# Kernel tuning notes

Measured on AMD Instinct MI355X. Metric: run time of the kernel, lower is better.

The kernel has to match this reference:

```python
import jax, jax.numpy as jnp
import numpy as np
from jax import lax

B, Hs, Ws = 2, 256, 256
DIM = 256        # query channels (c)
DIM_BAK = 256    # key/value channels (c2)
HEADS = 8
WIN = 8
HEAD_DIM = DIM // HEADS
SCALE = HEAD_DIM ** -0.5


def window_partition(x, ws):
    # x: [B, H, W, C] -> [B*nH*nW, ws, ws, C]
    b, h, w, c = x.shape
    x = x.reshape(b, h // ws, ws, w // ws, ws, c)
    return x.transpose(0, 1, 3, 2, 4, 5).reshape(-1, ws, ws, c)


def window_reverse(windows, ws, h, w):
    # windows: [B*nH*nW, ws, ws, C] -> [B, H, W, C]
    b = windows.shape[0] // ((h // ws) * (w // ws))
    x = windows.reshape(b, h // ws, w // ws, ws, ws, -1)
    return x.transpose(0, 1, 3, 2, 4, 5).reshape(b, h, w, -1)


def setup_inputs() -> dict:
    key = jax.random.key(0)
    ks = jax.random.split(key, 9)
    s = 0.02
    return {
        "query_feature": jax.random.normal(ks[0], (B, DIM, Hs, Ws), jnp.float32),
        "key_value_feature": jax.random.normal(ks[1], (B, DIM_BAK, Hs, Ws), jnp.float32),
        # depthwise 3x3 conv on kv (groups=DIM_BAK, bias=False): OIHW with I=1
        "w_dw": jax.random.normal(ks[2], (DIM_BAK, 1, 3, 3), jnp.float32) * s,
        # to_q: Linear(dim -> dim), stored [in, out]
        "wq": jax.random.normal(ks[3], (DIM, DIM), jnp.float32) * s,
        "bq": jax.random.normal(ks[4], (DIM,), jnp.float32) * s,
        # to_kv: Linear(dim_bak -> 2*dim)
        "wkv": jax.random.normal(ks[5], (DIM_BAK, 2 * DIM), jnp.float32) * s,
        "bkv": jax.random.normal(ks[6], (2 * DIM,), jnp.float32) * s,
        # project_out: Linear(dim -> dim)
        "w_proj": jax.random.normal(ks[7], (DIM, DIM), jnp.float32) * s,
        "b_proj": jax.random.normal(ks[8], (DIM,), jnp.float32) * s,
    }


def reference(query_feature, key_value_feature, w_dw, wq, bq, wkv, bkv, w_proj, b_proj):
    b, c, h, w = query_feature.shape
    c2 = key_value_feature.shape[1]

    # depthwise 3x3 conv on key/value feature (padding=1, stride=1)
    kv = lax.conv_general_dilated(
        key_value_feature, w_dw,
        window_strides=(1, 1), padding="SAME",
        feature_group_count=c2,
        dimension_numbers=("NCHW", "OIHW", "NCHW"))

    # NCHW -> NHWC, partition into non-overlapping windows
    qw = window_partition(query_feature.transpose(0, 2, 3, 1), WIN)  # [B_, ws, ws, c]
    kvw = window_partition(kv.transpose(0, 2, 3, 1), WIN)            # [B_, ws, ws, c2]
    B_ = qw.shape[0]
    N = WIN * WIN
    qw = qw.reshape(B_, N, c)
    kvw = kvw.reshape(B_, N, c2)

    # projections -> multi-head [B_, heads, N, head_dim]
    q = (qw @ wq + bq).reshape(B_, N, HEADS, HEAD_DIM).transpose(0, 2, 1, 3) * SCALE
    kv_proj = (kvw @ wkv + bkv).reshape(B_, N, 2, HEADS, HEAD_DIM)
    k = kv_proj[:, :, 0].transpose(0, 2, 1, 3)
    v = kv_proj[:, :, 1].transpose(0, 2, 1, 3)

    # windowed cross-attention
    attn = jax.nn.softmax(jnp.einsum("bhnd,bhmd->bhnm", q, k), axis=-1)
    out = jnp.einsum("bhnm,bhmd->bhnd", attn, v)
    out = out.transpose(0, 2, 1, 3).reshape(B_, N, c)
    out = out @ w_proj + b_proj

    # reverse windows, back to NCHW
    out = window_reverse(out.reshape(B_, WIN, WIN, c), WIN, h, w)
    return out.transpose(0, 3, 1, 2)
```

## Files before the change

### kernel.cpp

```cpp
#include <hip/hip_runtime.h>
#include <hip/hip_bf16.h>
#include <cstdint>
#include <cstddef>

typedef __hip_bfloat16 bf16;
typedef short bf16x8 __attribute__((ext_vector_type(8)));
typedef float f32x4 __attribute__((ext_vector_type(4)));

#define MFMA(a, b, c) __builtin_amdgcn_mfma_f32_16x16x32_bf16((a), (b), (c), 0, 0, 0)

__global__ __launch_bounds__(256) void wtrans_k(const float* __restrict__ wq,
                                                const float* __restrict__ wkv,
                                                const float* __restrict__ wp,
                                                bf16* __restrict__ wqT,
                                                bf16* __restrict__ wkvT,
                                                bf16* __restrict__ wpT) {
  int idx = blockIdx.x * 256 + threadIdx.x;
  if (idx < 65536) {
    int n = idx >> 8, k = idx & 255;
    wqT[idx] = __float2bfloat16(wq[k * 256 + n]);
  } else if (idx < 196608) {
    int i = idx - 65536;
    int n = i >> 8, k = i & 255;
    wkvT[i] = __float2bfloat16(wkv[k * 512 + n]);
  } else {
    int i = idx - 196608;
    int n = i >> 8, k = i & 255;
    wpT[i] = __float2bfloat16(wp[k * 256 + n]);
  }
}

__global__ __launch_bounds__(256) void t_winq_k(const float* __restrict__ src,
                                                bf16* __restrict__ dst,
                                                int hw0, int swoff) {
  __shared__ bf16 T[64][66];
  int tile = blockIdx.x;
  int c0 = (tile & 3) << 6;
  int hwb = hw0 + ((tile >> 2) << 6);
  int tid = threadIdx.x;
  {
    int hwl = tid & 63, cb = tid >> 6;
    const float* s = src + (size_t)(c0 + cb) * 65536 + hwb + hwl;
#pragma unroll
    for (int i = 0; i < 16; ++i)
      T[cb + i * 4][hwl] = __float2bfloat16(s[(size_t)i * 4 * 65536]);
  }
  __syncthreads();
  {
    int cl = tid & 63, hb = tid >> 6;
#pragma unroll
    for (int j = 0; j < 16; ++j) {
      int hwl = hb + j * 4;
      int hw = hwb + hwl;
      int h = hw >> 8, w = hw & 255;
      int sw = swoff + ((h >> 3) << 5) + (w >> 3);
      int t = ((h & 7) << 3) + (w & 7);
      dst[((size_t)(sw * 64 + t) << 8) + c0 + cl] = T[cl][hwl];
    }
  }
}

__global__ __launch_bounds__(256) void t_nhwc_k(const float* __restrict__ src,
                                                bf16* __restrict__ dst) {
  __shared__ bf16 T[64][66];
  int tile = blockIdx.x;
  int c0 = (tile & 3) << 6;
  int hwoff = (tile >> 2) << 6;
  int tid = threadIdx.x;
  {
    int hwl = tid & 63, cb = tid >> 6;
    const float* s = src + (size_t)(c0 + cb) * 65536 + hwoff + hwl;
#pragma unroll
    for (int i = 0; i < 16; ++i)
      T[cb + i * 4][hwl] = __float2bfloat16(s[(size_t)i * 4 * 65536]);
  }
  __syncthreads();
  {
    int cl = tid & 63, hb = tid >> 6;
#pragma unroll
    for (int j = 0; j < 16; ++j) {
      int hwl = hb + j * 4;
      dst[((size_t)(hwoff + hwl) << 8) + c0 + cl] = T[cl][hwl];
    }
  }
}

__global__ __launch_bounds__(256) void convkv_k(const bf16* __restrict__ SK,
                                                const float* __restrict__ wdw,
                                                const bf16* __restrict__ wkvT,
                                                const float* __restrict__ bkv,
                                                bf16* __restrict__ k_s,
                                                bf16* __restrict__ vT_s,
                                                int wid_base, int cnt, int psw0,
                                                int nwtot) {
  __shared__ __align__(16) bf16 X[64 * 256];
  auto xp = [&](int row, int col) -> bf16* {
    int by = (row << 9) + (col << 1);
    by ^= (row & 7) << 4;
    return (bf16*)((char*)X + by);
  };
  int bid = blockIdx.x;
  int swc = (bid & 7) * (cnt >> 3) + (bid >> 3);
  int sw = psw0 + swc;
  int wid = wid_base + swc;
  int rem = wid & 1023, wh = rem >> 5, ww = rem & 31;
  int h0 = wh * 8, w0 = ww * 8;
  int tid = threadIdx.x;
  {
    int c = tid;
    float wr[9];
#pragma unroll
    for (int q = 0; q < 9; ++q) wr[q] = wdw[c * 9 + q];
    const bool wlo = (w0 > 0), whi = (w0 < 248);
    float rows[3][10];
    auto load_row = [&](int gh, float* r) {
      if (gh >= 0 && gh < 256) {
        const bf16* rp = SK + ((size_t)(gh * 256 + w0) << 8) + c;
        r[0] = wlo ? __bfloat162float(rp[-256]) : 0.f;
#pragma unroll
        for (int s = 1; s <= 8; ++s) r[s] = __bfloat162float(rp[(s - 1) * 256]);
        r[9] = whi ? __bfloat162float(rp[8 * 256]) : 0.f;
      } else {
#pragma unroll
        for (int e = 0; e < 10; ++e) r[e] = 0.f;
      }
    };
    load_row(h0 - 1, rows[0]);
    load_row(h0, rows[1]);
#pragma unroll
    for (int i = 0; i < 8; ++i) {
      load_row(h0 + i + 1, rows[(i + 2) % 3]);
#pragma unroll
      for (int j = 0; j < 8; ++j) {
        float acc = 0.f;
#pragma unroll
        for (int di = 0; di < 3; ++di) {
          const float* rp = rows[(i + di) % 3];
          acc = __builtin_fmaf(wr[di * 3 + 0], rp[j], acc);
          acc = __builtin_fmaf(wr[di * 3 + 1], rp[j + 1], acc);
          acc = __builtin_fmaf(wr[di * 3 + 2], rp[j + 2], acc);
        }
        *xp(i * 8 + j, c) = __float2bfloat16(acc);
      }
    }
  }
  __syncthreads();
  int wave = tid >> 6, lane = tid & 63, quad = lane >> 4, l16 = lane & 15;
  int n0 = wave * 64;
  f32x4 zero4 = {0.f, 0.f, 0.f, 0.f};
  f32x4 acc[4][4];
  for (int mt = 0; mt < 4; ++mt)
    for (int nt = 0; nt < 4; ++nt) acc[mt][nt] = zero4;
  for (int k0 = 0; k0 < 256; k0 += 32) {
    bf16x8 a[4], bb[4];
    for (int mt = 0; mt < 4; ++mt)
      a[mt] = *(const bf16x8*)xp(mt * 16 + l16, k0 + quad * 8);
    for (int nt = 0; nt < 4; ++nt)
      bb[nt] = *(const bf16x8*)&wkvT[(size_t)(n0 + nt * 16 + l16) * 256 + k0 + quad * 8];
    for (int mt = 0; mt < 4; ++mt)
      for (int nt = 0; nt < 4; ++nt) acc[mt][nt] = MFMA(a[mt], bb[nt], acc[mt][nt]);
  }
  for (int nt = 0; nt < 4; ++nt) {
    int n = n0 + nt * 16 + l16;
    float bias = bkv[n];
    for (int mt = 0; mt < 4; ++mt) {
      int mb = mt * 16 + quad * 4;
      for (int r = 0; r < 4; ++r)
        k_s[((size_t)(sw * 64 + mb + r) << 8) + n] =
            __float2bfloat16(acc[mt][nt][r] + bias);
    }
  }
  for (int mt = 0; mt < 4; ++mt)
    for (int nt = 0; nt < 4; ++nt) acc[mt][nt] = zero4;
  for (int k0 = 0; k0 < 256; k0 += 32) {
    bf16x8 a[4], bb[4];
    for (int mt = 0; mt < 4; ++mt)
      a[mt] = *(const bf16x8*)xp(mt * 16 + l16, k0 + quad * 8);
    for (int nt = 0; nt < 4; ++nt)
      bb[nt] = *(const bf16x8*)&wkvT[(size_t)(256 + n0 + nt * 16 + l16) * 256 + k0 + quad * 8];
    for (int mt = 0; mt < 4; ++mt)
      for (int nt = 0; nt < 4; ++nt) acc[mt][nt] = MFMA(bb[nt], a[mt], acc[mt][nt]);
  }
  for (int nt = 0; nt < 4; ++nt) {
    for (int r = 0; r < 4; ++r) {
      int vd = n0 + nt * 16 + quad * 4 + r;
      float bias = bkv[256 + vd];
      for (int mt = 0; mt < 4; ++mt)
        vT_s[((size_t)(sw * 256 + vd) << 6) + mt * 16 + l16] =
            __float2bfloat16(acc[mt][nt][r] + bias);
    }
  }
}

__global__ __launch_bounds__(256, 2) void fused_k(const bf16* __restrict__ qwM,
                                                  const bf16* __restrict__ wqT,
                                                  const float* __restrict__ bq,
                                                  const bf16* __restrict__ k_s,
                                                  const bf16* __restrict__ vT_s,
                                                  const bf16* __restrict__ wpT,
                                                  const float* __restrict__ bp,
                                                  float* __restrict__ out,
                                                  int wid_base, int nw) {
  __shared__ __align__(16) bf16 XQ[64 * 256];
  __shared__ __align__(16) bf16 LA[4 * 64 * 64];
  int bid = blockIdx.x;
  int sw = (bid & 7) * (nw >> 3) + (bid >> 3);
  int wid = wid_base + sw;
  int b = wid >> 10, rem = wid & 1023, wh = rem >> 5, ww = rem & 31;
  int h0 = wh * 8, w0 = ww * 8;
  int tid = threadIdx.x, wave = tid >> 6, lane = tid & 63, quad = lane >> 4, l16 = lane & 15;
  const bf16* kw = k_s + ((size_t)sw << 14);
  const bf16* vw = vT_s + ((size_t)sw << 14);

  {
    const char* Aq = (const char*)(qwM + ((size_t)sw << 14));
#pragma unroll
    for (int rr = 0; rr < 8; ++rr) {
      int L = rr * 4096 + wave * 1024 + lane * 16;
      int gl = L ^ (((L >> 9) & 7) << 4);
      __builtin_amdgcn_global_load_lds(
          (const __attribute__((address_space(1))) void*)(Aq + gl),
          (__attribute__((address_space(3))) void*)((char*)XQ + rr * 4096 + wave * 1024),
          16, 0, 0);
    }
  }
  bf16x8 kfr[2][4], vfr[2][2][2];
#pragma unroll
  for (int hi = 0; hi < 2; ++hi) {
    int co = (wave + hi * 4) * 32;
#pragma unroll
    for (int nt = 0; nt < 4; ++nt)
      kfr[hi][nt] = *(const bf16x8*)&kw[(size_t)(nt * 16 + l16) * 256 + co + quad * 8];
#pragma unroll
    for (int half = 0; half < 2; ++half)
#pragma unroll
      for (int nt = 0; nt < 2; ++nt)
        vfr[hi][half][nt] =
            *(const bf16x8*)&vw[(size_t)(co + nt * 16 + l16) * 64 + half * 32 + quad * 8];
  }
  __syncthreads();

  auto xq = [&](int row, int col) -> const bf16* {
    int by = (row << 9) + (col << 1);
    by ^= (row & 7) << 4;
    return (const bf16*)((const char*)XQ + by);
  };
  char* Abase = (char*)LA + wave * 8192;
  auto ap = [&](int row, int col) -> bf16* {
    int by = (row << 7) + (col << 1);
    by ^= (row & 7) << 4;
    return (bf16*)(Abase + by);
  };
  auto apR = [&](int w, int row, int col) -> bf16* {
    int by = (row << 7) + (col << 1);
    by ^= (row & 7) << 4;
    return (bf16*)((char*)LA + w * 8192 + by);
  };
  f32x4 zero4 = {0.f, 0.f, 0.f, 0.f};

  {
    f32x4 acc[4][4];
    for (int mt = 0; mt < 4; ++mt)
      for (int nt = 0; nt < 4; ++nt) acc[mt][nt] = zero4;
    for (int k0 = 0; k0 < 256; k0 += 32) {
      bf16x8 a[4], bb[4];
      for (int mt = 0; mt < 4; ++mt)
        a[mt] = *(const bf16x8*)xq(mt * 16 + l16, k0 + quad * 8);
      for (int nt = 0; nt < 4; ++nt) {
        int n = (wave + ((nt >> 1) << 2)) * 32 + (nt & 1) * 16 + l16;
        bb[nt] = *(const bf16x8*)&wqT[(size_t)n * 256 + k0 + quad * 8];
      }
      for (int mt = 0; mt < 4; ++mt)
        for (int nt = 0; nt < 4; ++nt) acc[mt][nt] = MFMA(a[mt], bb[nt], acc[mt][nt]);
    }
    const float scale = 0.1767766952966369f;
    for (int nt = 0; nt < 4; ++nt) {
      int n = (wave + ((nt >> 1) << 2)) * 32 + (nt & 1) * 16 + l16;
      float bias = bq[n];
      for (int mt = 0; mt < 4; ++mt) {
        int mb = mt * 16 + quad * 4;
        for (int r = 0; r < 4; ++r)
          *ap(mb + r, nt * 16 + l16) =
              __float2bfloat16((acc[mt][nt][r] + bias) * scale);
      }
    }
  }
#pragma unroll
  for (int hi = 0; hi < 2; ++hi) {
    int lc = hi * 32;
    f32x4 s[4][4];
    for (int mt = 0; mt < 4; ++mt)
      for (int nt = 0; nt < 4; ++nt) s[mt][nt] = zero4;
    {
      bf16x8 a[4];
      for (int mt = 0; mt < 4; ++mt)
        a[mt] = *(const bf16x8*)ap(mt * 16 + l16, lc + quad * 8);
      for (int mt = 0; mt < 4; ++mt)
#pragma unroll
        for (int nt = 0; nt < 4; ++nt) s[mt][nt] = MFMA(a[mt], kfr[hi][nt], s[mt][nt]);
    }
    float rsum[4][4];
    for (int mt = 0; mt < 4; ++mt) {
      for (int r = 0; r < 4; ++r) {
        float m = s[mt][0][r];
        for (int nt = 1; nt < 4; ++nt) m = fmaxf(m, s[mt][nt][r]);
        m = fmaxf(m, __shfl_xor(m, 1, 64));
        m = fmaxf(m, __shfl_xor(m, 2, 64));
        m = fmaxf(m, __shfl_xor(m, 4, 64));
        m = fmaxf(m, __shfl_xor(m, 8, 64));
        float sum = 0.f;
        for (int nt = 0; nt < 4; ++nt) {
          float e = __expf(s[mt][nt][r] - m);
          s[mt][nt][r] = e;
          sum += e;
        }
        sum += __shfl_xor(sum, 1, 64);
        sum += __shfl_xor(sum, 2, 64);
        sum += __shfl_xor(sum, 4, 64);
        sum += __shfl_xor(sum, 8, 64);
        rsum[mt][r] = sum;
      }
    }
    f32x4 o[4][2];
    for (int mt = 0; mt < 4; ++mt)
      for (int nt = 0; nt < 2; ++nt) o[mt][nt] = zero4;
#pragma unroll
    for (int half = 0; half < 2; ++half) {
      for (int mt = 0; mt < 4; ++mt)
#pragma unroll
        for (int nt2 = 0; nt2 < 2; ++nt2)
          for (int r = 0; r < 4; ++r)
            *ap(mt * 16 + quad * 4 + r, lc + nt2 * 16 + l16) =
                __float2bfloat16(s[mt][half * 2 + nt2][r]);
      bf16x8 pa[4];
      for (int mt = 0; mt < 4; ++mt)
        pa[mt] = *(const bf16x8*)ap(mt * 16 + l16, lc + quad * 8);
      for (int mt = 0; mt < 4; ++mt)
#pragma unroll
        for (int nt = 0; nt < 2; ++nt)
          o[mt][nt] = MFMA(pa[mt], vfr[hi][half][nt], o[mt][nt]);
    }
    for (int mt = 0; mt < 4; ++mt) {
      int mb = mt * 16 + quad * 4;
      for (int nt = 0; nt < 2; ++nt)
        for (int r = 0; r < 4; ++r)
          *ap(mb + r, lc + nt * 16 + l16) =
              __float2bfloat16(o[mt][nt][r] / rsum[mt][r]);
    }
  }
  __syncthreads();
  {
    int n0 = wave * 64;
    f32x4 acc[4][4];
    for (int mt = 0; mt < 4; ++mt)
      for (int nt = 0; nt < 4; ++nt) acc[mt][nt] = zero4;
    for (int k0 = 0; k0 < 256; k0 += 32) {
      int head = k0 >> 5;
      int rw = head & 3;
      int lc = (head >> 2) * 32;
      bf16x8 a[4], bb[4];
      for (int mt = 0; mt < 4; ++mt)
        a[mt] = *(const bf16x8*)apR(rw, mt * 16 + l16, lc + quad * 8);
      for (int nt = 0; nt < 4; ++nt)
        bb[nt] = *(const bf16x8*)&wpT[(size_t)(n0 + nt * 16 + l16) * 256 + k0 + quad * 8];
      for (int mt = 0; mt < 4; ++mt)
        for (int nt = 0; nt < 4; ++nt) acc[mt][nt] = MFMA(a[mt], bb[nt], acc[mt][nt]);
    }
    for (int nt = 0; nt < 4; ++nt) {
      int n = n0 + nt * 16 + l16;
      float bias = bp[n];
      float* chan = out + ((size_t)(b * 256 + n) << 16);
      for (int mt = 0; mt < 4; ++mt) {
        int row_i = mt * 2 + (quad >> 1);
        int j0 = (quad & 1) * 4;
        f32x4 v4;
        for (int r = 0; r < 4; ++r) v4[r] = acc[mt][nt][r] + bias;
        *(f32x4*)&chan[(size_t)(h0 + row_i) * 256 + w0 + j0] = v4;
      }
    }
  }
}

extern "C" void kernel_launch(void* const* d_in, const int* in_sizes, int n_in,
                              void* d_out, int out_size, void* d_ws, size_t ws_size,
                              hipStream_t stream) {
  const float* qf  = (const float*)d_in[0];
  const float* kvf = (const float*)d_in[1];
  const float* wdw = (const float*)d_in[2];
  const float* wq  = (const float*)d_in[3];
  const float* bq  = (const float*)d_in[4];
  const float* wkv = (const float*)d_in[5];
  const float* bkv = (const float*)d_in[6];
  const float* wp  = (const float*)d_in[7];
  const float* bp  = (const float*)d_in[8];
  float* out = (float*)d_out;

  bf16* wqT  = (bf16*)d_ws;
  bf16* wkvT = wqT + 65536;
  bf16* wpT  = wkvT + 131072;
  bf16* bufs = wpT + 65536;
  const size_t welems = 65536 + 131072 + 65536;
  const size_t skelems = (size_t)256 * 256 * 256;

  int passes = 1;
  while (passes < 32) {
    size_t nw_ = 2048 / passes;
    size_t elems = welems + skelems + 3 * nw_ * 16384;
    if (elems * 2 <= ws_size) break;
    passes <<= 1;
  }
  int nw = 2048 / passes;
  size_t sz = (size_t)nw * 16384;
  bf16* SK  = bufs;
  bf16* qwM = SK + skelems;
  bf16* KS  = qwM + sz;
  bf16* VT  = KS + sz;

  wtrans_k<<<1024, 256, 0, stream>>>(wq, wkv, wp, wqT, wkvT, wpT);

  for (int p = 0; p < passes; ++p) {
    int wbP = p * nw;
    int b0 = wbP >> 10, b1 = (wbP + nw - 1) >> 10;
    for (int b = b0; b <= b1; ++b) {
      int s = wbP > b * 1024 ? wbP : b * 1024;
      int e = (wbP + nw) < (b + 1) * 1024 ? (wbP + nw) : (b + 1) * 1024;
      int cnt = e - s;
      int h0 = ((s & 1023) >> 5) * 8;
      t_winq_k<<<cnt * 4, 256, 0, stream>>>(qf + ((size_t)b << 24), qwM,
                                            h0 * 256, b * 1024 - wbP);
    }
    for (int b = b0; b <= b1; ++b) {
      int s = wbP > b * 1024 ? wbP : b * 1024;
      int e = (wbP + nw) < (b + 1) * 1024 ? (wbP + nw) : (b + 1) * 1024;
      int cnt = e - s;
      t_nhwc_k<<<4096, 256, 0, stream>>>(kvf + ((size_t)b << 24), SK);
      convkv_k<<<cnt, 256, 0, stream>>>(SK, wdw, wkvT, bkv, KS, VT,
                                        s, cnt, s - wbP, nw);
    }
    fused_k<<<nw, 256, 0, stream>>>(qwM, wqT, bq, KS, VT, wpT, bp, out, wbP, nw);
  }
}
```

Measured before the change: 595.5 us.

## Fuse depthwise conv and KV projection into attention kernel, keeping K/V in LDS

Merges the conv+KV-projection kernel with the fused attention kernel into one mega kernel, so K and V^T are written to shared memory instead of round-tripping through global buffers. The NHWC transposed kv buffer is now kept per batch, so both batches can be handled in a single pass. This removes the K/V global writes and reads and one launch per pass. In exchange it adds extra __syncthreads and drops the launch_bounds occupancy hint of 2. Per-block work also grows, which may reduce overlap.

```diff
diff --git a/kernel.cpp b/kernel.cpp
--- a/kernel.cpp
+++ b/kernel.cpp
@@ -85,27 +85,53 @@
   }
 }
 
-__global__ __launch_bounds__(256) void convkv_k(const bf16* __restrict__ SK,
-                                                const float* __restrict__ wdw,
-                                                const bf16* __restrict__ wkvT,
-                                                const float* __restrict__ bkv,
-                                                bf16* __restrict__ k_s,
-                                                bf16* __restrict__ vT_s,
-                                                int wid_base, int cnt, int psw0,
-                                                int nwtot) {
+__global__ __launch_bounds__(256) void mega_k(const bf16* __restrict__ SK,
+                                              const float* __restrict__ wdw,
+                                              const bf16* __restrict__ wkvT,
+                                              const float* __restrict__ bkv,
+                                              const bf16* __restrict__ qwM,
+                                              const bf16* __restrict__ wqT,
+                                              const float* __restrict__ bq,
+                                              const bf16* __restrict__ wpT,
+                                              const float* __restrict__ bp,
+                                              float* __restrict__ out,
+                                              int wid_base, int nw) {
   __shared__ __align__(16) bf16 X[64 * 256];
+  __shared__ __align__(16) bf16 LA[64 * 256];
+  int bid = blockIdx.x;
+  int sw = (bid & 7) * (nw >> 3) + (bid >> 3);
+  int wid = wid_base + sw;
+  int b = wid >> 10, rem = wid & 1023, wh = rem >> 5, ww = rem & 31;
+  int h0 = wh * 8, w0 = ww * 8;
+  int tid = threadIdx.x, wave = tid >> 6, lane = tid & 63, quad = lane >> 4, l16 = lane & 15;
+  const bf16* SKb = SK + (size_t)(b & 1) * 16777216;
   auto xp = [&](int row, int col) -> bf16* {
     int by = (row << 9) + (col << 1);
     by ^= (row & 7) << 4;
     return (bf16*)((char*)X + by);
   };
-  int bid = blockIdx.x;
-  int swc = (bid & 7) * (cnt >> 3) + (bid >> 3);
-  int sw = psw0 + swc;
-  int wid = wid_base + swc;
-  int rem = wid & 1023, wh = rem >> 5, ww = rem & 31;
-  int h0 = wh * 8, w0 = ww * 8;
-  int tid = threadIdx.x;
+  auto lak = [&](int row, int col) -> bf16* {
+    int by = (row << 9) + (col << 1);
+    by ^= (row & 7) << 4;
+    return (bf16*)((char*)LA + by);
+  };
+  auto lav = [&](int row, int col) -> bf16* {
+    int by = (row << 7) + (col << 1);
+    by ^= (row & 7) << 4;
+    return (bf16*)((char*)LA + by);
+  };
+  auto ap = [&](int row, int col) -> bf16* {
+    int by = (row << 7) + (col << 1);
+    by ^= (row & 7) << 4;
+    return (bf16*)((char*)LA + wave * 8192 + by);
+  };
+  auto apR = [&](int w, int row, int col) -> bf16* {
+    int by = (row << 7) + (col << 1);
+    by ^= (row & 7) << 4;
+    return (bf16*)((char*)LA + w * 8192 + by);
+  };
+  f32x4 zero4 = {0.f, 0.f, 0.f, 0.f};
+
   {
     int c = tid;
     float wr[9];
@@ -115,7 +141,7 @@
     float rows[3][10];
     auto load_row = [&](int gh, float* r) {
       if (gh >= 0 && gh < 256) {
-        const bf16* rp = SK + ((size_t)(gh * 256 + w0) << 8) + c;
+        const bf16* rp = SKb + ((size_t)(gh * 256 + w0) << 8) + c;
         r[0] = wlo ? __bfloat162float(rp[-256]) : 0.f;
 #pragma unroll
         for (int s = 1; s <= 8; ++s) r[s] = __bfloat162float(rp[(s - 1) * 256]);
@@ -145,33 +171,34 @@
     }
   }
   __syncthreads();
-  int wave = tid >> 6, lane = tid & 63, quad = lane >> 4, l16 = lane & 15;
+
   int n0 = wave * 64;
-  f32x4 zero4 = {0.f, 0.f, 0.f, 0.f};
-  f32x4 acc[4][4];
+  {
+    f32x4 kacc[4][4];
+    for (int mt = 0; mt < 4; ++mt)
+      for (int nt = 0; nt < 4; ++nt) kacc[mt][nt] = zero4;
+    for (int k0 = 0; k0 < 256; k0 += 32) {
+      bf16x8 a[4], bb[4];
+      for (int mt = 0; mt < 4; ++mt)
+        a[mt] = *(const bf16x8*)xp(mt * 16 + l16, k0 + quad * 8);
+      for (int nt = 0; nt < 4; ++nt)
+        bb[nt] = *(const bf16x8*)&wkvT[(size_t)(n0 + nt * 16 + l16) * 256 + k0 + quad * 8];
+      for (int mt = 0; mt < 4; ++mt)
+        for (int nt = 0; nt < 4; ++nt) kacc[mt][nt] = MFMA(a[mt], bb[nt], kacc[mt][nt]);
+    }
+    for (int nt = 0; nt < 4; ++nt) {
+      int n = n0 + nt * 16 + l16;
+      float bias = bkv[n];
+      for (int mt = 0; mt < 4; ++mt) {
+        int mb = mt * 16 + quad * 4;
+        for (int r = 0; r < 4; ++r)
+          *lak(mb + r, n) = __float2bfloat16(kacc[mt][nt][r] + bias);
+      }
+    }
+  }
+  f32x4 vacc[4][4];
   for (int mt = 0; mt < 4; ++mt)
-    for (int nt = 0; nt < 4; ++nt) acc[mt][nt] = zero4;
-  for (int k0 = 0; k0 < 256; k0 += 32) {
-    bf16x8 a[4], bb[4];
-    for (int mt = 0; mt < 4; ++mt)
-      a[mt] = *(const bf16x8*)xp(mt * 16 + l16, k0 + quad * 8);
-    for (int nt = 0; nt < 4; ++nt)
-      bb[nt] = *(const bf16x8*)&wkvT[(size_t)(n0 + nt * 16 + l16) * 256 + k0 + quad * 8];
-    for (int mt = 0; mt < 4; ++mt)
-      for (int nt = 0; nt < 4; ++nt) acc[mt][nt] = MFMA(a[mt], bb[nt], acc[mt][nt]);
-  }
-  for (int nt = 0; nt < 4; ++nt) {
-    int n = n0 + nt * 16 + l16;
-    float bias = bkv[n];
-    for (int mt = 0; mt < 4; ++mt) {
-      int mb = mt * 16 + quad * 4;
-      for (int r = 0; r < 4; ++r)
-        k_s[((size_t)(sw * 64 + mb + r) << 8) + n] =
-            __float2bfloat16(acc[mt][nt][r] + bias);
-    }
-  }
-  for (int mt = 0; mt < 4; ++mt)
-    for (int nt = 0; nt < 4; ++nt) acc[mt][nt] = zero4;
+    for (int nt = 0; nt < 4; ++nt) vacc[mt][nt] = zero4;
   for (int k0 = 0; k0 < 256; k0 += 32) {
     bf16x8 a[4], bb[4];
     for (int mt = 0; mt < 4; ++mt)
@@ -179,38 +206,9 @@
     for (int nt = 0; nt < 4; ++nt)
       bb[nt] = *(const bf16x8*)&wkvT[(size_t)(256 + n0 + nt * 16 + l16) * 256 + k0 + quad * 8];
     for (int mt = 0; mt < 4; ++mt)
-      for (int nt = 0; nt < 4; ++nt) acc[mt][nt] = MFMA(bb[nt], a[mt], acc[mt][nt]);
-  }
-  for (int nt = 0; nt < 4; ++nt) {
-    for (int r = 0; r < 4; ++r) {
-      int vd = n0 + nt * 16 + quad * 4 + r;
-      float bias = bkv[256 + vd];
-      for (int mt = 0; mt < 4; ++mt)
-        vT_s[((size_t)(sw * 256 + vd) << 6) + mt * 16 + l16] =
-            __float2bfloat16(acc[mt][nt][r] + bias);
-    }
-  }
-}
-
-__global__ __launch_bounds__(256, 2) void fused_k(const bf16* __restrict__ qwM,
-                                                  const bf16* __restrict__ wqT,
-                                                  const float* __restrict__ bq,
-                                                  const bf16* __restrict__ k_s,
-                                                  const bf16* __restrict__ vT_s,
-                                                  const bf16* __restrict__ wpT,
-                                                  const float* __restrict__ bp,
-                                                  float* __restrict__ out,
-                                                  int wid_base, int nw) {
-  __shared__ __align__(16) bf16 XQ[64 * 256];
-  __shared__ __align__(16) bf16 LA[4 * 64 * 64];
-  int bid = blockIdx.x;
-  int sw = (bid & 7) * (nw >> 3) + (bid >> 3);
-  int wid = wid_base + sw;
-  int b = wid >> 10, rem = wid & 1023, wh = rem >> 5, ww = rem & 31;
-  int h0 = wh * 8, w0 = ww * 8;
-  int tid = threadIdx.x, wave = tid >> 6, lane = tid & 63, quad = lane >> 4, l16 = lane & 15;
-  const bf16* kw = k_s + ((size_t)sw << 14);
-  const bf16* vw = vT_s + ((size_t)sw << 14);
+      for (int nt = 0; nt < 4; ++nt) vacc[mt][nt] = MFMA(bb[nt], a[mt], vacc[mt][nt]);
+  }
+  __syncthreads();
 
   {
     const char* Aq = (const char*)(qwM + ((size_t)sw << 14));
@@ -220,43 +218,41 @@
       int gl = L ^ (((L >> 9) & 7) << 4);
       __builtin_amdgcn_global_load_lds(
           (const __attribute__((address_space(1))) void*)(Aq + gl),
-          (__attribute__((address_space(3))) void*)((char*)XQ + rr * 4096 + wave * 1024),
+          (__attribute__((address_space(3))) void*)((char*)X + rr * 4096 + wave * 1024),
           16, 0, 0);
     }
   }
-  bf16x8 kfr[2][4], vfr[2][2][2];
+  bf16x8 kfr[2][4];
 #pragma unroll
   for (int hi = 0; hi < 2; ++hi) {
     int co = (wave + hi * 4) * 32;
 #pragma unroll
     for (int nt = 0; nt < 4; ++nt)
-      kfr[hi][nt] = *(const bf16x8*)&kw[(size_t)(nt * 16 + l16) * 256 + co + quad * 8];
+      kfr[hi][nt] = *(const bf16x8*)lak(nt * 16 + l16, co + quad * 8);
+  }
+  __syncthreads();
+
+  for (int nt = 0; nt < 4; ++nt) {
+    for (int r = 0; r < 4; ++r) {
+      int vd = n0 + nt * 16 + quad * 4 + r;
+      float bias = bkv[256 + vd];
+      for (int mt = 0; mt < 4; ++mt)
+        *lav(vd, mt * 16 + l16) = __float2bfloat16(vacc[mt][nt][r] + bias);
+    }
+  }
+  __syncthreads();
+
+  bf16x8 vfr[2][2][2];
+#pragma unroll
+  for (int hi = 0; hi < 2; ++hi) {
+    int co = (wave + hi * 4) * 32;
 #pragma unroll
     for (int half = 0; half < 2; ++half)
 #pragma unroll
       for (int nt = 0; nt < 2; ++nt)
-        vfr[hi][half][nt] =
-            *(const bf16x8*)&vw[(size_t)(co + nt * 16 + l16) * 64 + half * 32 + quad * 8];
-  }
-  __syncthreads();
-
-  auto xq = [&](int row, int col) -> const bf16* {
-    int by = (row << 9) + (col << 1);
-    by ^= (row & 7) << 4;
-    return (const bf16*)((const char*)XQ + by);
-  };
-  char* Abase = (char*)LA + wave * 8192;
-  auto ap = [&](int row, int col) -> bf16* {
-    int by = (row << 7) + (col << 1);
-    by ^= (row & 7) << 4;
-    return (bf16*)(Abase + by);
-  };
-  auto apR = [&](int w, int row, int col) -> bf16* {
-    int by = (row << 7) + (col << 1);
-    by ^= (row & 7) << 4;
-    return (bf16*)((char*)LA + w * 8192 + by);
-  };
-  f32x4 zero4 = {0.f, 0.f, 0.f, 0.f};
+        vfr[hi][half][nt] = *(const bf16x8*)lav(co + nt * 16 + l16, half * 32 + quad * 8);
+  }
+  __syncthreads();
 
   {
     f32x4 acc[4][4];
@@ -265,7 +261,7 @@
     for (int k0 = 0; k0 < 256; k0 += 32) {
       bf16x8 a[4], bb[4];
       for (int mt = 0; mt < 4; ++mt)
-        a[mt] = *(const bf16x8*)xq(mt * 16 + l16, k0 + quad * 8);
+        a[mt] = *(const bf16x8*)xp(mt * 16 + l16, k0 + quad * 8);
       for (int nt = 0; nt < 4; ++nt) {
         int n = (wave + ((nt >> 1) << 2)) * 32 + (nt & 1) * 16 + l16;
         bb[nt] = *(const bf16x8*)&wqT[(size_t)n * 256 + k0 + quad * 8];
@@ -350,7 +346,6 @@
   }
   __syncthreads();
   {
-    int n0 = wave * 64;
     f32x4 acc[4][4];
     for (int mt = 0; mt < 4; ++mt)
       for (int nt = 0; nt < 4; ++nt) acc[mt][nt] = zero4;
@@ -405,16 +400,13 @@
   int passes = 1;
   while (passes < 32) {
     size_t nw_ = 2048 / passes;
-    size_t elems = welems + skelems + 3 * nw_ * 16384;
+    size_t elems = welems + 2 * skelems + nw_ * 16384;
     if (elems * 2 <= ws_size) break;
     passes <<= 1;
   }
   int nw = 2048 / passes;
-  size_t sz = (size_t)nw * 16384;
   bf16* SK  = bufs;
-  bf16* qwM = SK + skelems;
-  bf16* KS  = qwM + sz;
-  bf16* VT  = KS + sz;
+  bf16* qwM = SK + 2 * skelems;
 
   wtrans_k<<<1024, 256, 0, stream>>>(wq, wkv, wp, wqT, wkvT, wpT);
 
@@ -428,15 +420,10 @@
       int h0 = ((s & 1023) >> 5) * 8;
       t_winq_k<<<cnt * 4, 256, 0, stream>>>(qf + ((size_t)b << 24), qwM,
                                             h0 * 256, b * 1024 - wbP);
-    }
-    for (int b = b0; b <= b1; ++b) {
-      int s = wbP > b * 1024 ? wbP : b * 1024;
-      int e = (wbP + nw) < (b + 1) * 1024 ? (wbP + nw) : (b + 1) * 1024;
-      int cnt = e - s;
-      t_nhwc_k<<<4096, 256, 0, stream>>>(kvf + ((size_t)b << 24), SK);
-      convkv_k<<<cnt, 256, 0, stream>>>(SK, wdw, wkvT, bkv, KS, VT,
-                                        s, cnt, s - wbP, nw);
-    }
-    fused_k<<<nw, 256, 0, stream>>>(qwM, wqT, bq, KS, VT, wpT, bp, out, wbP, nw);
+      t_nhwc_k<<<4096, 256, 0, stream>>>(kvf + ((size_t)b << 24),
+                                         SK + (size_t)(b & 1) * skelems);
+    }
+    mega_k<<<nw, 256, 0, stream>>>(SK, wdw, wkvT, bkv, qwM, wqT, bq, wpT, bp,
+                                   out, wbP, nw);
   }
 }
```

Result: slower. 651.4 us (+9.4%).
